# Kernel tuning notes

Hardware: AMD Instinct MI355X
Metric: run time of the kernel (lower is better)

The kernel has to match this reference:

```python
import jax, jax.numpy as jnp
import numpy as np

T, D, H, L = 8192, 1024, 1024, 4


def setup_inputs() -> dict:
    key = jax.random.key(0)
    ks = jax.random.split(key, 1 + 4 * L)
    lim = 1.0 / np.sqrt(H)  # equinox GRUCell uses U(-1/sqrt(hidden), 1/sqrt(hidden))
    inp = {"xs": jax.random.normal(ks[0], (T, D), dtype=jnp.float32)}
    in_sz = D
    for l in range(L):
        k0, k1, k2, k3 = ks[1 + 4 * l: 5 + 4 * l]
        inp[f"Wih{l}"] = jax.random.uniform(k0, (3 * H, in_sz), minval=-lim, maxval=lim, dtype=jnp.float32)
        inp[f"Whh{l}"] = jax.random.uniform(k1, (3 * H, H), minval=-lim, maxval=lim, dtype=jnp.float32)
        inp[f"b{l}"] = jax.random.uniform(k2, (3 * H,), minval=-lim, maxval=lim, dtype=jnp.float32)
        inp[f"bn{l}"] = jax.random.uniform(k3, (H,), minval=-lim, maxval=lim, dtype=jnp.float32)
        in_sz = H
    return inp


def _gru_layer(xs, Wih, Whh, b, bn):
    # Equinox GRUCell math: gates ordered (reset, update, new); h' = n + z*(h - n).
    Hd = Whh.shape[1]
    igates = xs @ Wih.T + b  # (T, 3H): input projections hoisted out of the scan

    def step(h, ig):
        hg = Whh @ h  # (3H,)
        r = jax.nn.sigmoid(ig[:Hd] + hg[:Hd])
        z = jax.nn.sigmoid(ig[Hd:2 * Hd] + hg[Hd:2 * Hd])
        n = jnp.tanh(ig[2 * Hd:] + r * (hg[2 * Hd:] + bn))
        h_new = n + z * (h - n)
        return h_new, h_new

    h0 = jnp.zeros((Hd,), dtype=xs.dtype)
    _, out = jax.lax.scan(step, h0, igates)
    return out  # (T, H)


def reference(xs, Wih0, Whh0, b0, bn0, Wih1, Whh1, b1, bn1,
              Wih2, Whh2, b2, bn2, Wih3, Whh3, b3, bn3):
    for Wih, Whh, b, bn in ((Wih0, Whh0, b0, bn0), (Wih1, Whh1, b1, bn1),
                            (Wih2, Whh2, b2, bn2), (Wih3, Whh3, b3, bn3)):
        xs = _gru_layer(xs, Wih, Whh, b, bn)
    return xs
```

## Files before the change

kernel.cpp:

```cpp
#include <hip/hip_runtime.h>

#define TSTEPS 8192
#define HDIM   1024
#define NLAYER 4
#define NB     256
#define NT     512
#define GB     64
#define EPB    16
#define RING   8

typedef float f32x4 __attribute__((ext_vector_type(4)));

struct GruParams {
  const float* xs;
  const float* Wih[NLAYER];
  const float* Whh[NLAYER];
  const float* bias[NLAYER];
  const float* bn[NLAYER];
  float* out;
  int*   tags;
  float* hbuf;
  float* ring;
};

__device__ __forceinline__ float sigmoidf_(float x) {
  return 1.0f / (1.0f + __expf(-x));
}
__device__ __forceinline__ float tanhf_(float x) {
  const float e = __expf(2.0f * x);
  return 1.0f - 2.0f / (e + 1.0f);
}
__device__ __forceinline__ float rfl_(float x) {
  return __int_as_float(__builtin_amdgcn_readfirstlane(__float_as_int(x)));
}

__device__ __forceinline__ void gather_row_(const float* row, float* lds,
                                            int lane) {
  const float* r0 = row + lane * 4;
  f32x4 a, b, c, d;
  asm volatile(
      "global_load_dwordx4 %0, %4, off sc1\n\t"
      "global_load_dwordx4 %1, %5, off sc1\n\t"
      "global_load_dwordx4 %2, %6, off sc1\n\t"
      "global_load_dwordx4 %3, %7, off sc1\n\t"
      "s_waitcnt vmcnt(0)"
      : "=&v"(a), "=&v"(b), "=&v"(c), "=&v"(d)
      : "v"(r0), "v"(r0 + 256), "v"(r0 + 512), "v"(r0 + 768)
      : "memory");
  *reinterpret_cast<f32x4*>(&lds[lane * 4 +   0]) = a;
  *reinterpret_cast<f32x4*>(&lds[lane * 4 + 256]) = b;
  *reinterpret_cast<f32x4*>(&lds[lane * 4 + 512]) = c;
  *reinterpret_cast<f32x4*>(&lds[lane * 4 + 768]) = d;
}

__global__ __attribute__((amdgpu_flat_work_group_size(NT, NT),
                          amdgpu_waves_per_eu(2, 2)))
void gru_pipe(GruParams p) {
  __shared__ float xst[HDIM];
  __shared__ float hst[HDIM];
  __shared__ float pad[19456];
  if ((size_t)p.out == 0) pad[threadIdx.x] = 0.f;

  const int tid  = threadIdx.x;
  const int lane = tid & 63;
  const int wave = tid >> 6;
  const int blk  = blockIdx.x;
  const int g    = blk >> 6;
  const int m    = blk & 63;
  const int j0   = m * EPB + wave * 2;

  const float* Wih = p.Wih[g];
  const float* Whh = p.Whh[g];
  f32x4 w4[48];
#pragma unroll
  for (int e = 0; e < 2; ++e) {
#pragma unroll
    for (int dd = 0; dd < 6; ++dd) {
      const float* W = (dd < 3) ? Wih : Whh;
      const int gate = (dd < 3) ? dd : dd - 3;
      const float* src = W + ((size_t)gate * HDIM + (j0 + e)) * HDIM + lane * 4;
#pragma unroll
      for (int i = 0; i < 4; ++i)
        w4[(e * 6 + dd) * 4 + i] = *reinterpret_cast<const f32x4*>(src + i * 256);
    }
  }
  const float bA0 = rfl_(p.bias[g][j0]);
  const float bA1 = rfl_(p.bias[g][HDIM + j0]);
  const float bA2 = rfl_(p.bias[g][2 * HDIM + j0]);
  const float bnA = rfl_(p.bn[g][j0]);
  const float bB0 = rfl_(p.bias[g][j0 + 1]);
  const float bB1 = rfl_(p.bias[g][HDIM + j0 + 1]);
  const float bB2 = rfl_(p.bias[g][2 * HDIM + j0 + 1]);
  const float bnB = rfl_(p.bn[g][j0 + 1]);
  float hregA = 0.f, hregB = 0.f;

  float* hb = p.hbuf + (size_t)g * 2 * HDIM;
  const float* ring_in  = p.ring + (size_t)(g - 1) * RING * HDIM;
  float*       ring_out = p.ring + (size_t)g * RING * HDIM;
  const int* ownp = p.tags + g * GB + lane;
  const int* upp  = (g > 0) ? (p.tags + (g - 1) * GB + lane) : ownp;
  const int* dwnp = (g < 3) ? (p.tags + (g + 1) * GB + lane) : ownp;

  for (int t = 0; t < TSTEPS; ++t) {
    if (wave == 0) {
      if (t > 0) {
        for (;;) {
          const int v = __hip_atomic_load(ownp, __ATOMIC_RELAXED,
                                          __HIP_MEMORY_SCOPE_AGENT);
          if (__all(v >= t)) break;
        }
        gather_row_(hb + (size_t)(t & 1) * HDIM, hst, lane);
      } else {
        const f32x4 z4 = {0.f, 0.f, 0.f, 0.f};
#pragma unroll
        for (int i = 0; i < 4; ++i)
          *reinterpret_cast<f32x4*>(&hst[lane * 4 + i * 256]) = z4;
      }
    } else if (wave == 1) {
      if (g > 0) {
        for (;;) {
          const int v = __hip_atomic_load(upp, __ATOMIC_RELAXED,
                                          __HIP_MEMORY_SCOPE_AGENT);
          if (__all(v >= t + 1)) break;
        }
        gather_row_(ring_in + (size_t)(t & (RING - 1)) * HDIM, xst, lane);
      } else {
        const float* xrow = p.xs + (size_t)t * HDIM + lane * 4;
#pragma unroll
        for (int i = 0; i < 4; ++i)
          *reinterpret_cast<f32x4*>(&xst[lane * 4 + i * 256]) =
              *reinterpret_cast<const f32x4*>(xrow + i * 256);
      }
    } else if (wave == 2) {
      if (g < 3 && t >= RING) {
        for (;;) {
          const int v = __hip_atomic_load(dwnp, __ATOMIC_RELAXED,
                                          __HIP_MEMORY_SCOPE_AGENT);
          if (__all(v >= t - (RING - 1))) break;
        }
      }
    }
    __syncthreads();

    float A_ir = 0.f, A_iz = 0.f, A_in = 0.f, A_hr = 0.f, A_hz = 0.f, A_hn = 0.f;
    float B_ir = 0.f, B_iz = 0.f, B_in = 0.f, B_hr = 0.f, B_hz = 0.f, B_hn = 0.f;
#pragma unroll
    for (int i = 0; i < 4; ++i) {
      const f32x4 xc = *reinterpret_cast<const f32x4*>(&xst[lane * 4 + i * 256]);
      const f32x4 hc = *reinterpret_cast<const f32x4*>(&hst[lane * 4 + i * 256]);
#pragma unroll
      for (int q = 0; q < 4; ++q) {
        const float xq = xc[q], hq = hc[q];
        A_ir = fmaf(w4[ 0 + i][q], xq, A_ir);
        A_iz = fmaf(w4[ 4 + i][q], xq, A_iz);
        A_in = fmaf(w4[ 8 + i][q], xq, A_in);
        A_hr = fmaf(w4[12 + i][q], hq, A_hr);
        A_hz = fmaf(w4[16 + i][q], hq, A_hz);
        A_hn = fmaf(w4[20 + i][q], hq, A_hn);
        B_ir = fmaf(w4[24 + i][q], xq, B_ir);
        B_iz = fmaf(w4[28 + i][q], xq, B_iz);
        B_in = fmaf(w4[32 + i][q], xq, B_in);
        B_hr = fmaf(w4[36 + i][q], hq, B_hr);
        B_hz = fmaf(w4[40 + i][q], hq, B_hz);
        B_hn = fmaf(w4[44 + i][q], hq, B_hn);
      }
    }
    float sAr = A_ir + A_hr, sAz = A_iz + A_hz;
    float sBr = B_ir + B_hr, sBz = B_iz + B_hz;
#pragma unroll
    for (int off = 32; off > 0; off >>= 1) {
      sAr  += __shfl_xor(sAr,  off, 64);
      sAz  += __shfl_xor(sAz,  off, 64);
      A_in += __shfl_xor(A_in, off, 64);
      A_hn += __shfl_xor(A_hn, off, 64);
      sBr  += __shfl_xor(sBr,  off, 64);
      sBz  += __shfl_xor(sBz,  off, 64);
      B_in += __shfl_xor(B_in, off, 64);
      B_hn += __shfl_xor(B_hn, off, 64);
    }

    const float rA = sigmoidf_(sAr + bA0);
    const float zA = sigmoidf_(sAz + bA1);
    const float nA = tanhf_(A_in + bA2 + rA * (A_hn + bnA));
    const float hA = nA + zA * (hregA - nA);
    const float rB = sigmoidf_(sBr + bB0);
    const float zB = sigmoidf_(sBz + bB1);
    const float nB = tanhf_(B_in + bB2 + rB * (B_hn + bnB));
    const float hB = nB + zB * (hregB - nB);
    hregA = hA; hregB = hB;

    if (lane == 0) {
      const unsigned long long pk =
          ((unsigned long long)__float_as_uint(hB) << 32) |
          (unsigned long long)__float_as_uint(hA);
      float* hdst = hb + (size_t)((t + 1) & 1) * HDIM + j0;
      asm volatile("global_store_dwordx2 %0, %1, off sc1"
                   :: "v"(hdst), "v"(pk) : "memory");
      float* xdst = (g < 3)
          ? ring_out + (size_t)(t & (RING - 1)) * HDIM + j0
          : p.out + (size_t)t * HDIM + j0;
      asm volatile("global_store_dwordx2 %0, %1, off sc1"
                   :: "v"(xdst), "v"(pk) : "memory");
    }
    asm volatile("s_waitcnt vmcnt(0)" ::: "memory");
    __syncthreads();
    if (tid == 0)
      __hip_atomic_store(&p.tags[blk], t + 1,
                         __ATOMIC_RELAXED, __HIP_MEMORY_SCOPE_AGENT);
  }
}

extern "C" void kernel_launch(void* const* d_in, const int* in_sizes, int n_in,
                              void* d_out, int out_size, void* d_ws, size_t ws_size,
                              hipStream_t stream) {
  GruParams p;
  p.xs = (const float*)d_in[0];
  for (int l = 0; l < NLAYER; ++l) {
    p.Wih[l]  = (const float*)d_in[1 + 4 * l];
    p.Whh[l]  = (const float*)d_in[2 + 4 * l];
    p.bias[l] = (const float*)d_in[3 + 4 * l];
    p.bn[l]   = (const float*)d_in[4 + 4 * l];
  }
  char* ws = (char*)d_ws;
  size_t off = 0;
  p.tags = (int*)(ws + off);
  off += (size_t)NB * sizeof(int);
  off = (off + 255) & ~(size_t)255;
  p.hbuf = (float*)(ws + off);
  off += (size_t)NLAYER * 2 * HDIM * sizeof(float);
  p.ring = (float*)(ws + off);
  off += (size_t)3 * RING * HDIM * sizeof(float);
  p.out = (float*)d_out;

  (void)hipMemsetAsync(p.tags, 0, (size_t)NB * sizeof(int), stream);
  gru_pipe<<<dim3(NB), dim3(NT), 0, stream>>>(p);
}
```

Measured before the change: 44.03 ms.

## Embed step tags in data words and overlap input projection with hidden-state polling

After: 39.03 ms. 11.4% less time.

```diff
diff --git a/kernel.cpp b/kernel.cpp
--- a/kernel.cpp
+++ b/kernel.cpp
@@ -7,9 +7,11 @@
 #define NT     512
 #define GB     64
 #define EPB    16
-#define RING   8
-
-typedef float f32x4 __attribute__((ext_vector_type(4)));
+#define RING   16
+
+typedef float    f32x4 __attribute__((ext_vector_type(4)));
+typedef unsigned u32x4 __attribute__((ext_vector_type(4)));
+typedef unsigned long long u64;
 
 struct GruParams {
   const float* xs;
@@ -18,9 +20,9 @@
   const float* bias[NLAYER];
   const float* bn[NLAYER];
   float* out;
-  int*   tags;
-  float* hbuf;
-  float* ring;
+  int*   ctags;
+  u64*   hbp;
+  u64*   ringp;
 };
 
 __device__ __forceinline__ float sigmoidf_(float x) {
@@ -34,33 +36,62 @@
   return __int_as_float(__builtin_amdgcn_readfirstlane(__float_as_int(x)));
 }
 
-__device__ __forceinline__ void gather_row_(const float* row, float* lds,
-                                            int lane) {
-  const float* r0 = row + lane * 4;
-  f32x4 a, b, c, d;
-  asm volatile(
-      "global_load_dwordx4 %0, %4, off sc1\n\t"
-      "global_load_dwordx4 %1, %5, off sc1\n\t"
-      "global_load_dwordx4 %2, %6, off sc1\n\t"
-      "global_load_dwordx4 %3, %7, off sc1\n\t"
-      "s_waitcnt vmcnt(0)"
-      : "=&v"(a), "=&v"(b), "=&v"(c), "=&v"(d)
-      : "v"(r0), "v"(r0 + 256), "v"(r0 + 512), "v"(r0 + 768)
-      : "memory");
-  *reinterpret_cast<f32x4*>(&lds[lane * 4 +   0]) = a;
-  *reinterpret_cast<f32x4*>(&lds[lane * 4 + 256]) = b;
-  *reinterpret_cast<f32x4*>(&lds[lane * 4 + 512]) = c;
-  *reinterpret_cast<f32x4*>(&lds[lane * 4 + 768]) = d;
+__device__ __forceinline__ void poll_stage_row_(const u64* buf, unsigned e,
+                                                float* lds, int lane) {
+  const u64* p0 = buf + lane * 4;
+  u32x4 r0, r1, r2, r3, r4, r5, r6, r7;
+  for (;;) {
+    asm volatile(
+        "global_load_dwordx4 %0, %8, off sc1\n\t"
+        "global_load_dwordx4 %1, %9, off sc1\n\t"
+        "global_load_dwordx4 %2, %10, off sc1\n\t"
+        "global_load_dwordx4 %3, %11, off sc1\n\t"
+        "global_load_dwordx4 %4, %12, off sc1\n\t"
+        "global_load_dwordx4 %5, %13, off sc1\n\t"
+        "global_load_dwordx4 %6, %14, off sc1\n\t"
+        "global_load_dwordx4 %7, %15, off sc1\n\t"
+        "s_waitcnt vmcnt(0)"
+        : "=&v"(r0), "=&v"(r1), "=&v"(r2), "=&v"(r3),
+          "=&v"(r4), "=&v"(r5), "=&v"(r6), "=&v"(r7)
+        : "v"(p0), "v"(p0 + 2), "v"(p0 + 256), "v"(p0 + 258),
+          "v"(p0 + 512), "v"(p0 + 514), "v"(p0 + 768), "v"(p0 + 770)
+        : "memory");
+    bool ok = (r0.y == e) & (r0.w == e) & (r1.y == e) & (r1.w == e) &
+              (r2.y == e) & (r2.w == e) & (r3.y == e) & (r3.w == e) &
+              (r4.y == e) & (r4.w == e) & (r5.y == e) & (r5.w == e) &
+              (r6.y == e) & (r6.w == e) & (r7.y == e) & (r7.w == e);
+    if (__all(ok)) break;
+    __builtin_amdgcn_s_sleep(1);
+  }
+  f32x4 v;
+  v.x = __uint_as_float(r0.x); v.y = __uint_as_float(r0.z);
+  v.z = __uint_as_float(r1.x); v.w = __uint_as_float(r1.z);
+  *reinterpret_cast<f32x4*>(&lds[0 * 256 + lane * 4]) = v;
+  v.x = __uint_as_float(r2.x); v.y = __uint_as_float(r2.z);
+  v.z = __uint_as_float(r3.x); v.w = __uint_as_float(r3.z);
+  *reinterpret_cast<f32x4*>(&lds[1 * 256 + lane * 4]) = v;
+  v.x = __uint_as_float(r4.x); v.y = __uint_as_float(r4.z);
+  v.z = __uint_as_float(r5.x); v.w = __uint_as_float(r5.z);
+  *reinterpret_cast<f32x4*>(&lds[2 * 256 + lane * 4]) = v;
+  v.x = __uint_as_float(r6.x); v.y = __uint_as_float(r6.z);
+  v.z = __uint_as_float(r7.x); v.w = __uint_as_float(r7.z);
+  *reinterpret_cast<f32x4*>(&lds[3 * 256 + lane * 4]) = v;
+}
+
+__device__ __forceinline__ void stage_plain_row_(const float* row, float* lds,
+                                                 int lane) {
+#pragma unroll
+  for (int i = 0; i < 4; ++i)
+    *reinterpret_cast<f32x4*>(&lds[i * 256 + lane * 4]) =
+        *reinterpret_cast<const f32x4*>(row + i * 256 + lane * 4);
 }
 
 __global__ __attribute__((amdgpu_flat_work_group_size(NT, NT),
                           amdgpu_waves_per_eu(2, 2)))
 void gru_pipe(GruParams p) {
-  __shared__ float xst[HDIM];
-  __shared__ float hst[HDIM];
-  __shared__ float pad[19456];
-  if ((size_t)p.out == 0) pad[threadIdx.x] = 0.f;
-
+  __shared__ float xst[2][HDIM];
+  __shared__ float hst[2][HDIM];
+  __shared__ int hflag[2];
   const int tid  = threadIdx.x;
   const int lane = tid & 63;
   const int wave = tid >> 6;
@@ -94,77 +125,99 @@
   const float bnB = rfl_(p.bn[g][j0 + 1]);
   float hregA = 0.f, hregB = 0.f;
 
-  float* hb = p.hbuf + (size_t)g * 2 * HDIM;
-  const float* ring_in  = p.ring + (size_t)(g - 1) * RING * HDIM;
-  float*       ring_out = p.ring + (size_t)g * RING * HDIM;
-  const int* ownp = p.tags + g * GB + lane;
-  const int* upp  = (g > 0) ? (p.tags + (g - 1) * GB + lane) : ownp;
-  const int* dwnp = (g < 3) ? (p.tags + (g + 1) * GB + lane) : ownp;
+  u64* hp = p.hbp + (size_t)g * 2 * HDIM;
+  const u64* ring_in  = p.ringp + (size_t)(g - 1) * RING * HDIM;
+  u64*       ring_out = p.ringp + (size_t)g * RING * HDIM;
+
+  if (tid == 0) { hflag[0] = -1; hflag[1] = -1; }
+  if (wave == 1) {
+    if (g == 0)
+      stage_plain_row_(p.xs, &xst[0][0], lane);
+    else {
+      poll_stage_row_(ring_in, 1u, &xst[0][0], lane);
+      if (lane == 0)
+        __hip_atomic_store(&p.ctags[blk], 1, __ATOMIC_RELAXED,
+                           __HIP_MEMORY_SCOPE_AGENT);
+    }
+  }
+  __syncthreads();
 
   for (int t = 0; t < TSTEPS; ++t) {
-    if (wave == 0) {
-      if (t > 0) {
-        for (;;) {
-          const int v = __hip_atomic_load(ownp, __ATOMIC_RELAXED,
-                                          __HIP_MEMORY_SCOPE_AGENT);
-          if (__all(v >= t)) break;
-        }
-        gather_row_(hb + (size_t)(t & 1) * HDIM, hst, lane);
-      } else {
-        const f32x4 z4 = {0.f, 0.f, 0.f, 0.f};
-#pragma unroll
-        for (int i = 0; i < 4; ++i)
-          *reinterpret_cast<f32x4*>(&hst[lane * 4 + i * 256]) = z4;
-      }
-    } else if (wave == 1) {
-      if (g > 0) {
-        for (;;) {
-          const int v = __hip_atomic_load(upp, __ATOMIC_RELAXED,
-                                          __HIP_MEMORY_SCOPE_AGENT);
-          if (__all(v >= t + 1)) break;
-        }
-        gather_row_(ring_in + (size_t)(t & (RING - 1)) * HDIM, xst, lane);
-      } else {
-        const float* xrow = p.xs + (size_t)t * HDIM + lane * 4;
-#pragma unroll
-        for (int i = 0; i < 4; ++i)
-          *reinterpret_cast<f32x4*>(&xst[lane * 4 + i * 256]) =
-              *reinterpret_cast<const f32x4*>(xrow + i * 256);
-      }
-    } else if (wave == 2) {
-      if (g < 3 && t >= RING) {
-        for (;;) {
-          const int v = __hip_atomic_load(dwnp, __ATOMIC_RELAXED,
-                                          __HIP_MEMORY_SCOPE_AGENT);
-          if (__all(v >= t - (RING - 1))) break;
-        }
-      }
-    }
-    __syncthreads();
-
-    float A_ir = 0.f, A_iz = 0.f, A_in = 0.f, A_hr = 0.f, A_hz = 0.f, A_hn = 0.f;
-    float B_ir = 0.f, B_iz = 0.f, B_in = 0.f, B_hr = 0.f, B_hz = 0.f, B_hn = 0.f;
+    const int par = t & 1;
+
+    float A_ir = 0.f, A_iz = 0.f, A_in = 0.f;
+    float B_ir = 0.f, B_iz = 0.f, B_in = 0.f;
 #pragma unroll
     for (int i = 0; i < 4; ++i) {
-      const f32x4 xc = *reinterpret_cast<const f32x4*>(&xst[lane * 4 + i * 256]);
-      const f32x4 hc = *reinterpret_cast<const f32x4*>(&hst[lane * 4 + i * 256]);
+      const f32x4 v = *reinterpret_cast<const f32x4*>(&xst[par][i * 256 + lane * 4]);
 #pragma unroll
       for (int q = 0; q < 4; ++q) {
-        const float xq = xc[q], hq = hc[q];
+        const float xq = v[q];
         A_ir = fmaf(w4[ 0 + i][q], xq, A_ir);
         A_iz = fmaf(w4[ 4 + i][q], xq, A_iz);
         A_in = fmaf(w4[ 8 + i][q], xq, A_in);
-        A_hr = fmaf(w4[12 + i][q], hq, A_hr);
-        A_hz = fmaf(w4[16 + i][q], hq, A_hz);
-        A_hn = fmaf(w4[20 + i][q], hq, A_hn);
         B_ir = fmaf(w4[24 + i][q], xq, B_ir);
         B_iz = fmaf(w4[28 + i][q], xq, B_iz);
         B_in = fmaf(w4[32 + i][q], xq, B_in);
-        B_hr = fmaf(w4[36 + i][q], hq, B_hr);
-        B_hz = fmaf(w4[40 + i][q], hq, B_hz);
-        B_hn = fmaf(w4[44 + i][q], hq, B_hn);
-      }
-    }
+      }
+    }
+
+    if (wave == 0) {
+      if (t > 0) {
+        poll_stage_row_(hp + (size_t)par * HDIM, (unsigned)t, &hst[par][0], lane);
+        asm volatile("s_waitcnt lgkmcnt(0)" ::: "memory");
+        if (lane == 0) ((volatile int*)hflag)[par] = t;
+      }
+    } else if (wave == 1) {
+      if (t + 1 < TSTEPS) {
+        const int pn = (t + 1) & 1;
+        if (g == 0)
+          stage_plain_row_(p.xs + (size_t)(t + 1) * HDIM, &xst[pn][0], lane);
+        else {
+          poll_stage_row_(ring_in + (size_t)((t + 1) & (RING - 1)) * HDIM,
+                          (unsigned)(t + 2), &xst[pn][0], lane);
+          if (lane == 0)
+            __hip_atomic_store(&p.ctags[blk], t + 2, __ATOMIC_RELAXED,
+                               __HIP_MEMORY_SCOPE_AGENT);
+        }
+      }
+    } else if (wave == 2) {
+      if (g < 3 && t >= RING && (t & 7) == 0) {
+        const int bound = t - 8;
+        const int* tp = p.ctags + (g + 1) * GB + lane;
+        for (;;) {
+          const int v = __hip_atomic_load(tp, __ATOMIC_RELAXED,
+                                          __HIP_MEMORY_SCOPE_AGENT);
+          if (__all(v >= bound)) break;
+          __builtin_amdgcn_s_sleep(4);
+        }
+      }
+    }
+
+    float A_hr = 0.f, A_hz = 0.f, A_hn = 0.f;
+    float B_hr = 0.f, B_hz = 0.f, B_hn = 0.f;
+    if (t > 0) {
+      if (wave != 0) {
+        while (((volatile int*)hflag)[par] != t) { }
+        asm volatile("s_waitcnt lgkmcnt(0)" ::: "memory");
+        __builtin_amdgcn_sched_barrier(0);
+      }
+#pragma unroll
+      for (int i = 0; i < 4; ++i) {
+        const f32x4 v = *reinterpret_cast<const f32x4*>(&hst[par][i * 256 + lane * 4]);
+#pragma unroll
+        for (int q = 0; q < 4; ++q) {
+          const float hq = v[q];
+          A_hr = fmaf(w4[12 + i][q], hq, A_hr);
+          A_hz = fmaf(w4[16 + i][q], hq, A_hz);
+          A_hn = fmaf(w4[20 + i][q], hq, A_hn);
+          B_hr = fmaf(w4[36 + i][q], hq, B_hr);
+          B_hz = fmaf(w4[40 + i][q], hq, B_hz);
+          B_hn = fmaf(w4[44 + i][q], hq, B_hn);
+        }
+      }
+    }
+
     float sAr = A_ir + A_hr, sAz = A_iz + A_hz;
     float sBr = B_ir + B_hr, sBz = B_iz + B_hz;
 #pragma unroll
@@ -178,7 +231,6 @@
       B_in += __shfl_xor(B_in, off, 64);
       B_hn += __shfl_xor(B_hn, off, 64);
     }
-
     const float rA = sigmoidf_(sAr + bA0);
     const float zA = sigmoidf_(sAz + bA1);
     const float nA = tanhf_(A_in + bA2 + rA * (A_hn + bnA));
@@ -190,23 +242,25 @@
     hregA = hA; hregB = hB;
 
     if (lane == 0) {
-      const unsigned long long pk =
-          ((unsigned long long)__float_as_uint(hB) << 32) |
-          (unsigned long long)__float_as_uint(hA);
-      float* hdst = hb + (size_t)((t + 1) & 1) * HDIM + j0;
-      asm volatile("global_store_dwordx2 %0, %1, off sc1"
+      u32x4 pk;
+      pk.x = __float_as_uint(hA); pk.y = (unsigned)(t + 1);
+      pk.z = __float_as_uint(hB); pk.w = (unsigned)(t + 1);
+      u64* hdst = hp + (size_t)((t + 1) & 1) * HDIM + j0;
+      asm volatile("global_store_dwordx4 %0, %1, off sc1"
                    :: "v"(hdst), "v"(pk) : "memory");
-      float* xdst = (g < 3)
-          ? ring_out + (size_t)(t & (RING - 1)) * HDIM + j0
-          : p.out + (size_t)t * HDIM + j0;
-      asm volatile("global_store_dwordx2 %0, %1, off sc1"
-                   :: "v"(xdst), "v"(pk) : "memory");
-    }
-    asm volatile("s_waitcnt vmcnt(0)" ::: "memory");
+      if (g < 3) {
+        u64* rdst = ring_out + (size_t)(t & (RING - 1)) * HDIM + j0;
+        asm volatile("global_store_dwordx4 %0, %1, off sc1"
+                     :: "v"(rdst), "v"(pk) : "memory");
+      } else {
+        const u64 po = ((u64)__float_as_uint(hB) << 32) |
+                       (u64)__float_as_uint(hA);
+        float* od = p.out + (size_t)t * HDIM + j0;
+        asm volatile("global_store_dwordx2 %0, %1, off sc1"
+                     :: "v"(od), "v"(po) : "memory");
+      }
+    }
     __syncthreads();
-    if (tid == 0)
-      __hip_atomic_store(&p.tags[blk], t + 1,
-                         __ATOMIC_RELAXED, __HIP_MEMORY_SCOPE_AGENT);
   }
 }
 
@@ -223,15 +277,19 @@
   }
   char* ws = (char*)d_ws;
   size_t off = 0;
-  p.tags = (int*)(ws + off);
+  p.ctags = (int*)(ws + off);
   off += (size_t)NB * sizeof(int);
   off = (off + 255) & ~(size_t)255;
-  p.hbuf = (float*)(ws + off);
-  off += (size_t)NLAYER * 2 * HDIM * sizeof(float);
-  p.ring = (float*)(ws + off);
-  off += (size_t)3 * RING * HDIM * sizeof(float);
+  p.hbp = (u64*)(ws + off);
+  const size_t hbp_bytes = (size_t)NLAYER * 2 * HDIM * sizeof(u64);
+  off += hbp_bytes;
+  p.ringp = (u64*)(ws + off);
+  const size_t ring_bytes = (size_t)3 * RING * HDIM * sizeof(u64);
+  off += ring_bytes;
   p.out = (float*)d_out;
 
-  (void)hipMemsetAsync(p.tags, 0, (size_t)NB * sizeof(int), stream);
+  (void)hipMemsetAsync(p.ctags, 0, (size_t)NB * sizeof(int), stream);
+  (void)hipMemsetAsync(p.hbp, 0, hbp_bytes, stream);
+  (void)hipMemsetAsync(p.ringp, 0, ring_bytes, stream);
   gru_pipe<<<dim3(NB), dim3(NT), 0, stream>>>(p);
 }
```
